# Optimization experiments

Hardware: AMD Instinct MI355X
Metric: run time of the kernel (lower is better)

Reference implementation:

```python
import jax, jax.numpy as jnp
import numpy as np

N, H, L, S, E, D = 2, 8, 2048, 2048, 64, 64
C, K, BITS, ITERS = 128, 32, 32, 10
TEMP = 1.0 / np.sqrt(E)  # softmax_temp default 1/sqrt(E)


def setup_inputs() -> dict:
    key = jax.random.key(0)
    k1, k2, k3, k4 = jax.random.split(key, 4)
    return {
        "queries": jax.random.normal(k1, (N, L, H, E), jnp.float32),
        "keys": jax.random.normal(k2, (N, S, H, E), jnp.float32),
        "values": jax.random.normal(k3, (N, S, H, D), jnp.float32),
        "planes": jax.random.normal(k4, (BITS, E + 1), jnp.float32),
    }


def _cluster(bits):
    """K-means (Lloyd) on hamming distance over hash bits. bits: [N,H,L,B] in {0,1}."""
    qsum = bits.sum(-1)  # [N,H,L]
    idx0 = jnp.linspace(0, L - 1, C).astype(jnp.int32)  # deterministic centroid init
    cbits0 = bits[:, :, idx0, :]  # [N,H,C,B]

    def assign(cbits):
        # hamming(x,c) = sum(x) + sum(c) - 2*x.c  for 0/1 bits
        d = qsum[..., None] + cbits.sum(-1)[:, :, None, :] \
            - 2.0 * jnp.einsum('nhlb,nhcb->nhlc', bits, cbits)
        return jnp.argmin(d, -1)  # [N,H,L]

    def body(cbits, _):
        cl = assign(cbits)
        oh = jax.nn.one_hot(cl, C, dtype=bits.dtype)       # [N,H,L,C]
        counts = oh.sum(2)                                  # [N,H,C]
        bs = jnp.einsum('nhlc,nhlb->nhcb', oh, bits)        # per-cluster bit sums
        newc = (2.0 * bs > counts[..., None]).astype(bits.dtype)  # majority vote
        newc = jnp.where(counts[..., None] > 0, newc, cbits)      # keep empty clusters
        return newc, None

    cbits, _ = jax.lax.scan(body, cbits0, None, length=ITERS)
    cl = assign(cbits)
    counts = jax.nn.one_hot(cl, C, dtype=jnp.float32).sum(2)
    return cl, counts


def reference(queries, keys, values, planes):
    q = queries.transpose(0, 2, 1, 3)  # [N,H,L,E]
    k = keys.transpose(0, 2, 1, 3)     # [N,H,S,E]
    v = values.transpose(0, 2, 1, 3)   # [N,H,S,D]

    # LSH hashing of queries
    proj = jnp.einsum('nhle,be->nhlb', q, planes[:, :E]) + planes[:, E]
    bits = (proj > 0).astype(jnp.float32)
    cl, counts = _cluster(bits)  # [N,H,L], [N,H,C]

    sorted_indx = jnp.argsort(cl, axis=-1)
    sorted_cl = jnp.take_along_axis(cl, sorted_indx, -1)
    sq = jnp.take_along_axis(q, sorted_indx[..., None], 2)  # queries sorted by cluster

    # grouped queries = per-cluster mean
    counts_safe = jnp.maximum(counts, 1.0)
    oh = jax.nn.one_hot(cl, C, dtype=q.dtype)
    Qg = jnp.einsum('nhlc,nhle->nhce', oh, q) / counts_safe[..., None]

    # centroid-key dot products and top-k key selection per cluster
    QK = jnp.einsum('nhce,nhse->nhcs', Qg, k)  # [N,H,C,S]
    topk_values, topk = jax.lax.top_k(QK, K)   # [N,H,C,K]

    # bottom-k attention (dense per-cluster, top-k positions zeroed)
    A_full = jax.nn.softmax(TEMP * QK, -1)
    iN = jnp.arange(N)[:, None, None, None]
    iH = jnp.arange(H)[None, :, None, None]
    iC = jnp.arange(C)[None, None, :, None]
    mask = jnp.zeros_like(QK).at[iN, iH, iC, topk].set(1.0)
    A_b = A_full * (1.0 - mask)
    A_bottomk = A_b.sum(-1)                              # [N,H,C]
    Vb_g = jnp.einsum('nhcs,nhsd->nhcd', A_b, v)         # [N,H,C,D]
    Vb = jnp.take_along_axis(Vb_g, sorted_cl[..., None], 2)   # broadcast to queries
    A_bk_q = jnp.take_along_axis(A_bottomk, sorted_cl, 2)     # [N,H,L]

    # exact top-k attention per query
    topk_q = jnp.take_along_axis(topk, sorted_cl[..., None], 2)  # [N,H,L,K]
    gather = jax.vmap(jax.vmap(lambda t, i: t[i]))  # over N,H
    K_sel = gather(k, topk_q)  # [N,H,L,K,E]
    V_sel = gather(v, topk_q)  # [N,H,L,K,D]
    QKs = jnp.einsum('nhle,nhlke->nhlk', sq, K_sel)
    inf_mask = jnp.isinf(topk_values[:, 0, 0, :])  # [N,K] (padding sentinel; all False here)
    QKs = jnp.where(inf_mask[:, None, None, :], -jnp.inf, QKs)
    A_s = jax.nn.softmax(TEMP * QKs, -1) * (1.0 - A_bk_q[..., None])
    Vt = jnp.einsum('nhlk,nhlkd->nhld', A_s, V_sel)

    # combine and undo the cluster sort
    Vs = Vt + Vb
    rev = jnp.argsort(sorted_indx, -1)
    V_new = jnp.take_along_axis(Vs, rev[..., None], 2)
    sparse_index = jnp.take_along_axis(topk_q, rev[..., None], 2)
    A_topk = jnp.take_along_axis(A_s, rev[..., None], 2)
    return V_new.transpose(0, 2, 1, 3), sparse_index, A_topk
```

## Files before the change

### kernel.cpp

```cpp
#include <hip/hip_runtime.h>
#include <math.h>

constexpr int cN = 2, cH = 8, cL = 2048, cS = 2048, cE = 64, cD = 64;
constexpr int cC = 128, cK = 32, cB = 32, cIT = 10;
constexpr int cNH = cN * cH;
constexpr int SK = 8;
constexpr int CHUNK = cS / SK;
constexpr int NT = 8;
constexpr int HW = cC * 33;
constexpr int NBUF = cIT + 1;

__global__ __launch_bounds__(256)
void k_bits(const float* __restrict__ q, const float* __restrict__ planes,
            unsigned int* __restrict__ bits, int* __restrict__ ghist)
{
    __shared__ float pl[cB * 68];
    int tid = threadIdx.x;
    for (int i = tid; i < cB * (cE + 1); i += 256) {
        int b = i / 65, e = i % 65;
        pl[b * 68 + e] = planes[i];
    }
    {
        const int ZS = NBUF * cNH * HW / 128;
        for (int i = tid; i < ZS; i += 256) ghist[(size_t)blockIdx.x * ZS + i] = 0;
    }
    __syncthreads();
    int idx = blockIdx.x * 256 + tid;
    int l = idx % cL, h = (idx / cL) % cH, n = idx / (cL * cH);
    const float* qr = q + (((size_t)n * cL + l) * cH + h) * cE;
    float qv[cE];
#pragma unroll
    for (int e4 = 0; e4 < cE / 4; ++e4) {
        float4 f = ((const float4*)qr)[e4];
        qv[4*e4+0] = f.x; qv[4*e4+1] = f.y; qv[4*e4+2] = f.z; qv[4*e4+3] = f.w;
    }
    unsigned int w = 0;
    for (int b = 0; b < cB; ++b) {
        const float4* pr = (const float4*)(pl + b * 68);
        float acc = 0.f;
#pragma unroll
        for (int e4 = 0; e4 < cE / 4; ++e4) {
            float4 f = pr[e4];
            acc = fmaf(qv[4*e4+0], f.x, acc);
            acc = fmaf(qv[4*e4+1], f.y, acc);
            acc = fmaf(qv[4*e4+2], f.z, acc);
            acc = fmaf(qv[4*e4+3], f.w, acc);
        }
        acc += pl[b * 68 + 64];
        if (acc > 0.f) w |= (1u << b);
    }
    bits[idx] = w;
}

__global__ __launch_bounds__(256)
void k_lloyd(const unsigned int* __restrict__ bits, int* __restrict__ ghist,
             unsigned int* __restrict__ cents, int* __restrict__ cl,
             int* __restrict__ pcounts, int it)
{
    __shared__ unsigned int scb[cC] __attribute__((aligned(16)));
    __shared__ int hist[HW];
    int tid = threadIdx.x, lane = tid & 63;
    int tile = blockIdx.x & (NT - 1), nh = blockIdx.x / NT;
    if (it == 0) {
        if (tid < cC) {
            int i0 = (int)(((double)tid * 2047.0) / 127.0);
            scb[tid] = bits[(size_t)nh * cL + i0];
        }
    } else {
        const unsigned int* cp = cents + (size_t)(it - 1) * cNH * cC + nh * cC;
        const int* gb = ghist + (size_t)((it - 1) * cNH + nh) * HW;
        if (tid < cC) {
            unsigned int oldc = cp[tid];
            int cnt = gb[4096 + tid];
            if (cnt > 0) {
                unsigned int nw = 0;
#pragma unroll
                for (int b = 0; b < cB; ++b)
                    if (2 * gb[tid * 32 + b] > cnt) nw |= (1u << b);
                oldc = nw;
            }
            scb[tid] = oldc;
        }
    }
    if (it < cIT) {
        for (int i = tid; i < HW; i += 256) hist[i] = 0;
    } else {
        if (tid < cC) hist[4096 + tid] = 0;
    }
    int l = tile * 256 + tid;
    unsigned int w = bits[(size_t)nh * cL + l];
    unsigned long long mymb = 0ull;
    if (it < cIT) {
#pragma unroll
        for (int b = 0; b < cB; ++b) {
            unsigned long long m = __ballot((w >> b) & 1u);
            if ((lane & 31) == b) mymb = m;
        }
    }
    __syncthreads();
    if (tile == 0 && it < cIT && tid < cC)
        cents[(size_t)it * cNH * cC + nh * cC + tid] = scb[tid];
    const uint4* scb4 = (const uint4*)scb;
    int b0 = 0x7fffffff, b1 = 0x7fffffff, b2 = 0x7fffffff, b3 = 0x7fffffff;
    for (int c4 = 0; c4 < cC / 4; ++c4) {
        uint4 cb = scb4[c4];
        int c = c4 * 4;
        b0 = min(b0, (__popc(w ^ cb.x) << 8) | c);
        b1 = min(b1, (__popc(w ^ cb.y) << 8) | (c + 1));
        b2 = min(b2, (__popc(w ^ cb.z) << 8) | (c + 2));
        b3 = min(b3, (__popc(w ^ cb.w) << 8) | (c + 3));
    }
    int best = min(min(b0, b1), min(b2, b3));
    int bc = best & 255;
    if (it == cIT) cl[(size_t)nh * cL + l] = bc;
    if (it < cIT) {
        unsigned long long rem = ~0ull;
        while (rem) {
            int src = __ffsll((long long)rem) - 1;
            int c = __shfl(bc, src);
            unsigned long long m = __ballot(bc == c);
            if (lane < cB) {
                int contrib = __popcll(m & mymb);
                if (contrib) atomicAdd(&hist[c * 32 + lane], contrib);
            }
            if (lane == 63) atomicAdd(&hist[4096 + c], __popcll(m));
            rem &= ~m;
        }
        __syncthreads();
        int* gb = ghist + (size_t)(it * cNH + nh) * HW;
        for (int i = tid; i < HW; i += 256) {
            int v = hist[i];
            if (v) atomicAdd(&gb[i], v);
        }
    } else {
        unsigned long long rem = ~0ull;
        while (rem) {
            int src = __ffsll((long long)rem) - 1;
            int c = __shfl(bc, src);
            unsigned long long m = __ballot(bc == c);
            if (lane == 63) atomicAdd(&hist[4096 + c], __popcll(m));
            rem &= ~m;
        }
        __syncthreads();
        if (tid < cC) pcounts[(nh * NT + tile) * cC + tid] = hist[4096 + tid];
    }
}

__global__ __launch_bounds__(256)
void k_rank(const int* __restrict__ cl, const int* __restrict__ pcounts,
            int* __restrict__ counts, int* __restrict__ moff,
            int* __restrict__ mlist)
{
    __shared__ int pre[cC];
    __shared__ int scn[cC];
    __shared__ int sbefore[cC];
    __shared__ int wcnt[4][cC];
    int tid = threadIdx.x, lane = tid & 63, wid = tid >> 6;
    int tile = blockIdx.x & (NT - 1), nh = blockIdx.x / NT;
    if (tid < cC) {
        int tot = 0, bef = 0;
        for (int t = 0; t < NT; ++t) {
            int v = pcounts[(nh * NT + t) * cC + tid];
            if (t < tile) bef += v;
            tot += v;
        }
        scn[tid] = tot;
        sbefore[tid] = bef;
    }
    {
        int* wf = &wcnt[0][0];
        for (int i = tid; i < 4 * cC; i += 256) wf[i] = 0;
    }
    __syncthreads();
    if (tid == 0) {
        int run = 0;
        for (int i = 0; i < cC; ++i) { pre[i] = run; run += scn[i]; }
    }
    __syncthreads();
    if (tile == 0) {
        if (tid < cC) {
            counts[nh * cC + tid] = scn[tid];
            moff[nh * cC + tid] = pre[tid];
        }
    }
    int l = tile * 256 + tid;
    int bc = cl[(size_t)nh * cL + l];
    unsigned long long ltmask = (1ull << lane) - 1ull;
    int myrank = 0;
    {
        unsigned long long rem = ~0ull;
        while (rem) {
            int src = __ffsll((long long)rem) - 1;
            int c = __shfl(bc, src);
            unsigned long long m = __ballot(bc == c);
            if (lane == 0) wcnt[wid][c] = __popcll(m);
            if (bc == c) myrank = __popcll(m & ltmask);
            rem &= ~m;
        }
    }
    __syncthreads();
    int off = pre[bc] + sbefore[bc] + myrank;
    for (int w2 = 0; w2 < 4; ++w2)
        if (w2 < wid) off += wcnt[w2][bc];
    mlist[(size_t)nh * cL + off] = l;
}

__global__ __launch_bounds__(64)
void k_qg(const float* __restrict__ q, const int* __restrict__ mlist,
          const int* __restrict__ moff, const int* __restrict__ counts,
          float* __restrict__ Qg)
{
    int b = blockIdx.x;
    int nh = b >> 7;
    int h = nh % cH, n = nh / cH;
    int lane = threadIdx.x;
    int off = moff[b];
    int cnt = counts[b];
    const int* ml = mlist + (size_t)nh * cL + off;
    const float* qb = q + ((size_t)n * cL * cH + h) * cE + lane;
    float acc = 0.f;
    int j = 0;
    for (; j + 4 <= cnt; j += 4) {
        int i0 = ml[j], i1 = ml[j + 1], i2 = ml[j + 2], i3 = ml[j + 3];
        float v0 = qb[(size_t)i0 * cH * cE];
        float v1 = qb[(size_t)i1 * cH * cE];
        float v2 = qb[(size_t)i2 * cH * cE];
        float v3 = qb[(size_t)i3 * cH * cE];
        acc += v0; acc += v1; acc += v2; acc += v3;
    }
    for (; j < cnt; ++j) acc += qb[(size_t)ml[j] * cH * cE];
    float cs = (float)(cnt > 0 ? cnt : 1);
    Qg[(size_t)b * cE + lane] = acc / cs;
}

__global__ __launch_bounds__(256)
void k_qk_gemm(const float* __restrict__ key, const float* __restrict__ Qg,
               float* __restrict__ QK)
{
    __shared__ float qgT[cE][cC + 2];
    __shared__ float kT[cE][128 + 2];
    int tid = threadIdx.x;
    int bs = blockIdx.x & 15;
    int nh = blockIdx.x >> 4;
    int h = nh % cH, n = nh / cH;
    const float4* qsrc = (const float4*)(Qg + (size_t)nh * cC * cE);
#pragma unroll
    for (int i = 0; i < 8; ++i) {
        int f = tid + 256 * i;
        int c = f >> 4, e4 = (f & 15) << 2;
        float4 v = qsrc[f];
        qgT[e4+0][c] = v.x; qgT[e4+1][c] = v.y; qgT[e4+2][c] = v.z; qgT[e4+3][c] = v.w;
    }
    const float* kb = key + (size_t)n * cS * cH * cE + (size_t)h * cE;
    int s0 = bs * 128;
#pragma unroll
    for (int i = 0; i < 8; ++i) {
        int f = tid + 256 * i;
        int s = f >> 4, e4 = (f & 15) << 2;
        float4 v = *(const float4*)(kb + (size_t)(s0 + s) * (cH * cE) + e4);
        kT[e4+0][s] = v.x; kT[e4+1][s] = v.y; kT[e4+2][s] = v.z; kT[e4+3][s] = v.w;
    }
    __syncthreads();
    int tx = tid & 15, ty = tid >> 4;
    float acc[8][8];
#pragma unroll
    for (int i = 0; i < 8; ++i)
#pragma unroll
        for (int j = 0; j < 8; ++j) acc[i][j] = 0.f;
    for (int e = 0; e < cE; ++e) {
        float qv[8], kv[8];
#pragma unroll
        for (int i = 0; i < 8; ++i) qv[i] = qgT[e][ty + 16 * i];
#pragma unroll
        for (int j = 0; j < 8; ++j) kv[j] = kT[e][tx + 16 * j];
#pragma unroll
        for (int i = 0; i < 8; ++i)
#pragma unroll
            for (int j = 0; j < 8; ++j)
                acc[i][j] = fmaf(qv[i], kv[j], acc[i][j]);
    }
    float* dst = QK + (size_t)nh * cC * cS + s0;
#pragma unroll
    for (int i = 0; i < 8; ++i)
#pragma unroll
        for (int j = 0; j < 8; ++j)
            dst[(size_t)(ty + 16 * i) * cS + tx + 16 * j] = acc[i][j];
}

__global__ __launch_bounds__(256)
void k_sel(float* __restrict__ QK, int* __restrict__ topk,
           float* __restrict__ abk)
{
    __shared__ int sbins[4 * 257];
    __shared__ int ired[4];
    __shared__ float fred[4];
    __shared__ unsigned skey[cK];
    __shared__ float sval[cK];
    __shared__ int sidx[cK];
    __shared__ int stopk[cK];
    __shared__ int sDig, sRem, scnt;
    __shared__ float sM;
    int tid = threadIdx.x, lane = tid & 63, wid = tid >> 6;
    int b = blockIdx.x;
    float* qrow = QK + (size_t)b * cS;
    float v[8]; unsigned key[8];
#pragma unroll
    for (int j = 0; j < 8; ++j) {
        float f = qrow[tid + j * 256];
        v[j] = f;
        unsigned u = __float_as_uint(f);
        key[j] = (u & 0x80000000u) ? ~u : (u | 0x80000000u);
    }
    if (tid == 0) { sRem = cK; scnt = 0; }
    unsigned pfx = 0;
    for (int pass = 0; pass < 4; ++pass) {
        int sh = 24 - 8 * pass;
        for (int i = tid; i < 4 * 257; i += 256) sbins[i] = 0;
        __syncthreads();
        int rem = sRem;
#pragma unroll
        for (int j = 0; j < 8; ++j) {
            bool cand = (pass == 0) || ((key[j] >> (sh + 8)) == pfx);
            if (cand) atomicAdd(&sbins[wid * 257 + ((key[j] >> sh) & 255)], 1);
        }
        __syncthreads();
        if (wid == 0) {
            int d0 = lane * 4;
            int c0 = sbins[d0] + sbins[257 + d0] + sbins[514 + d0] + sbins[771 + d0];
            int c1 = sbins[d0+1] + sbins[257+d0+1] + sbins[514+d0+1] + sbins[771+d0+1];
            int c2 = sbins[d0+2] + sbins[257+d0+2] + sbins[514+d0+2] + sbins[771+d0+2];
            int c3 = sbins[d0+3] + sbins[257+d0+3] + sbins[514+d0+3] + sbins[771+d0+3];
            int tot = c0 + c1 + c2 + c3;
            int incl = tot;
#pragma unroll
            for (int off = 1; off < 64; off <<= 1) {
                int o = __shfl_down(incl, off);
                if (lane + off < 64) incl += o;
            }
            int sufHi = incl - tot;
            int G3 = sufHi, G2 = sufHi + c3, G1 = G2 + c2, G0 = G1 + c1;
            int hit = -1, hG = 0;
            if (G0 < rem && rem <= G0 + c0) { hit = d0 + 0; hG = G0; }
            if (G1 < rem && rem <= G1 + c1) { hit = d0 + 1; hG = G1; }
            if (G2 < rem && rem <= G2 + c2) { hit = d0 + 2; hG = G2; }
            if (G3 < rem && rem <= G3 + c3) { hit = d0 + 3; hG = G3; }
            unsigned long long m = __ballot(hit >= 0);
            int src = __ffsll((long long)m) - 1;
            int dsel = __shfl(hit, src);
            int Gsel = __shfl(hG, src);
            if (lane == 0) { sDig = dsel; sRem = rem - Gsel; }
        }
        __syncthreads();
        pfx = (pfx << 8) | (unsigned)sDig;
    }
    unsigned T = pfx;
    int need = sRem;
    int myT = 0;
#pragma unroll
    for (int j = 0; j < 8; ++j) myT += (key[j] == T);
#pragma unroll
    for (int off = 1; off < 64; off <<= 1) myT += __shfl_xor(myT, off);
    if (lane == 0) ired[wid] = myT;
    __syncthreads();
    int tieTot = ((ired[0] + ired[1]) + ired[2]) + ired[3];
    int tieCut = 0x7fffffff;
    if (tieTot != need) {
        int last = -1;
        for (int t = 0; t < need; ++t) {
            int mymin = 0x7fffffff;
#pragma unroll
            for (int j = 0; j < 8; ++j) {
                int idx = tid + j * 256;
                if (key[j] == T && idx > last) mymin = min(mymin, idx);
            }
#pragma unroll
            for (int off = 1; off < 64; off <<= 1)
                mymin = min(mymin, __shfl_xor(mymin, off));
            __syncthreads();
            if (lane == 0) ired[wid] = mymin;
            __syncthreads();
            last = min(min(ired[0], ired[1]), min(ired[2], ired[3]));
        }
        tieCut = last;
    }
    __syncthreads();
    int selm = 0;
#pragma unroll
    for (int j = 0; j < 8; ++j) {
        int idx = tid + j * 256;
        bool s_ = (key[j] > T) || (key[j] == T && idx <= tieCut);
        if (s_) {
            int slot = atomicAdd(&scnt, 1);
            skey[slot] = key[j]; sidx[slot] = idx; sval[slot] = v[j];
            selm |= (1 << j);
        }
    }
    __syncthreads();
    if (tid < cK) {
        unsigned kt = skey[tid]; int it = sidx[tid];
        int rank = 0;
#pragma unroll
        for (int j = 0; j < cK; ++j)
            rank += (skey[j] > kt) || (skey[j] == kt && sidx[j] < it);
        stopk[rank] = it;
        if (rank == 0) sM = sval[tid];
    }
    __syncthreads();
    if (tid < cK) topk[(size_t)b * cK + tid] = stopk[tid];
    float M = sM;
    float e8[8]; float ps = 0.f;
#pragma unroll
    for (int j = 0; j < 8; ++j) { e8[j] = expf(0.125f * (v[j] - M)); ps += e8[j]; }
#pragma unroll
    for (int off = 1; off < 64; off <<= 1) ps += __shfl_xor(ps, off);
    if (lane == 0) fred[wid] = ps;
    __syncthreads();
    float den = ((fred[0] + fred[1]) + fred[2]) + fred[3];
    float ab = 0.f;
#pragma unroll
    for (int j = 0; j < 8; ++j) {
        float P = (selm & (1 << j)) ? 0.f : e8[j] / den;
        ab += P;
        qrow[tid + j * 256] = P;
    }
#pragma unroll
    for (int off = 1; off < 64; off <<= 1) ab += __shfl_xor(ab, off);
    __syncthreads();
    if (lane == 0) fred[wid] = ab;
    __syncthreads();
    if (tid == 0) abk[b] = ((fred[0] + fred[1]) + fred[2]) + fred[3];
}

__global__ __launch_bounds__(256)
void k_pv(const float* __restrict__ P, const float* __restrict__ val,
          float* __restrict__ part)
{
    __shared__ float pT[64][64 + 2];
    __shared__ float vT[64][cD + 4];
    int tid = threadIdx.x;
    int ch = blockIdx.x & 1;
    int sk = (blockIdx.x >> 1) & 7;
    int nh = blockIdx.x >> 4;
    int h = nh % cH, n = nh / cH;
    int tx = tid & 15, ty = tid >> 4;
    float acc[4][4];
#pragma unroll
    for (int i = 0; i < 4; ++i)
#pragma unroll
        for (int j = 0; j < 4; ++j) acc[i][j] = 0.f;
    const float* pb = P + ((size_t)nh * cC + ch * 64) * cS;
    const float* vb = val + (size_t)n * cS * cH * cD + (size_t)h * cD;
    for (int sub = 0; sub < CHUNK / 64; ++sub) {
        int s0 = sk * CHUNK + sub * 64;
#pragma unroll
        for (int i = 0; i < 4; ++i) {
            int f = tid + 256 * i;
            int c = f >> 4, s4 = (f & 15) << 2;
            float4 v = *(const float4*)(pb + (size_t)c * cS + s0 + s4);
            pT[c][s4+0] = v.x; pT[c][s4+1] = v.y; pT[c][s4+2] = v.z; pT[c][s4+3] = v.w;
        }
#pragma unroll
        for (int i = 0; i < 4; ++i) {
            int f = tid + 256 * i;
            int ss = f >> 4, d4 = (f & 15) << 2;
            float4 v = *(const float4*)(vb + (size_t)(s0 + ss) * (cH * cD) + d4);
            vT[ss][d4+0] = v.x; vT[ss][d4+1] = v.y; vT[ss][d4+2] = v.z; vT[ss][d4+3] = v.w;
        }
        __syncthreads();
        for (int ss = 0; ss < 64; ++ss) {
            float pv[4];
#pragma unroll
            for (int i = 0; i < 4; ++i) pv[i] = pT[ty + 16 * i][ss];
            float4 vv = *(const float4*)&vT[ss][tx * 4];
#pragma unroll
            for (int i = 0; i < 4; ++i) {
                acc[i][0] = fmaf(pv[i], vv.x, acc[i][0]);
                acc[i][1] = fmaf(pv[i], vv.y, acc[i][1]);
                acc[i][2] = fmaf(pv[i], vv.z, acc[i][2]);
                acc[i][3] = fmaf(pv[i], vv.w, acc[i][3]);
            }
        }
        __syncthreads();
    }
    float* dst = part + (((size_t)sk * cNH + nh) * cC + ch * 64) * cD;
#pragma unroll
    for (int i = 0; i < 4; ++i) {
        float4 o; o.x = acc[i][0]; o.y = acc[i][1]; o.z = acc[i][2]; o.w = acc[i][3];
        *(float4*)(dst + (size_t)(ty + 16 * i) * cD + tx * 4) = o;
    }
}

__global__ __launch_bounds__(256)
void k_out(const float* __restrict__ q, const float* __restrict__ key,
           const float* __restrict__ val, const int* __restrict__ mlist,
           const int* __restrict__ moff, const int* __restrict__ counts,
           const float* __restrict__ abk, const float* __restrict__ part,
           const int* __restrict__ topk, float* __restrict__ out)
{
    __shared__ float vlds[cK][cD + 1];
    __shared__ float aslds[4][cK];
    __shared__ int   st[cK];
    int tid = threadIdx.x, lane = tid & 63, wid = tid >> 6;
    int b = blockIdx.x;
    int nh = b >> 7;
    int h = nh % cH, n = nh / cH;
    if (tid < cK) st[tid] = topk[(size_t)b * cK + tid];
    __syncthreads();
    const float* kb = key + ((size_t)n * cS * cH + h) * cE;
    const float* vb = val + ((size_t)n * cS * cH + h) * cD;
    for (int r = wid; r < cK; r += 4)
        vlds[r][lane] = vb[(size_t)st[r] * cH * cD + lane];
    int k = lane >> 1, hh = lane & 1;
    float4 kreg[8];
    {
        const float* kr = kb + (size_t)st[k] * cH * cE + hh * 32;
#pragma unroll
        for (int j = 0; j < 8; ++j) kreg[j] = ((const float4*)kr)[j];
    }
    float vbgd = 0.f;
    {
        const float* pp = part + (size_t)b * cD + lane;
#pragma unroll
        for (int sk = 0; sk < SK; ++sk)
            vbgd += pp[(size_t)sk * (cNH * cC * cD)];
    }
    __syncthreads();
    int cnt = counts[b];
    int off = moff[b];
    float scale = 1.0f - abk[b];
    float stf = (lane < cK) ? (float)st[lane] : 0.f;
    const int* ml = mlist + (size_t)nh * cL + off;
    const size_t off1 = (size_t)cN * cL * cH * cD;
    const size_t off2 = off1 + (size_t)cN * cH * cL * cK;
    for (int m = wid; m < cnt; m += 4) {
        int l = ml[m];
        const float* qrow = q + (((size_t)n * cL + l) * cH + h) * cE + hh * 32;
        float4 qf[8];
#pragma unroll
        for (int j = 0; j < 8; ++j) qf[j] = ((const float4*)qrow)[j];
        float partial = 0.f;
#pragma unroll
        for (int j = 0; j < 8; ++j) {
            partial = fmaf(qf[j].x, kreg[j].x, partial);
            partial = fmaf(qf[j].y, kreg[j].y, partial);
            partial = fmaf(qf[j].z, kreg[j].z, partial);
            partial = fmaf(qf[j].w, kreg[j].w, partial);
        }
        float qk = partial + __shfl_xor(partial, 1);
        float M = qk;
#pragma unroll
        for (int o = 2; o < 64; o <<= 1) M = fmaxf(M, __shfl_xor(M, o));
        float ev = expf(0.125f * (qk - M));
        float den = ev;
#pragma unroll
        for (int o = 2; o < 64; o <<= 1) den += __shfl_xor(den, o);
        float as_ = (ev / den) * scale;
        if (!hh) aslds[wid][k] = as_;
        float acc = 0.f;
#pragma unroll
        for (int j = 0; j < cK; ++j)
            acc = fmaf(aslds[wid][j], vlds[j][lane], acc);
        acc += vbgd;
        int qidx = nh * cL + l;
        out[(((size_t)n * cL + l) * cH + h) * cD + lane] = acc;
        if (lane < cK) {
            out[off1 + (size_t)qidx * cK + lane] = stf;
            out[off2 + (size_t)qidx * cK + lane] = aslds[wid][lane];
        }
    }
}

extern "C" void kernel_launch(void* const* d_in, const int* in_sizes, int n_in,
                              void* d_out, int out_size, void* d_ws, size_t ws_size,
                              hipStream_t stream)
{
    (void)in_sizes; (void)n_in; (void)out_size; (void)ws_size;
    const float* q      = (const float*)d_in[0];
    const float* key    = (const float*)d_in[1];
    const float* val    = (const float*)d_in[2];
    const float* planes = (const float*)d_in[3];
    char* w = (char*)d_ws;
    unsigned int* bits = (unsigned int*)w;  w += (size_t)cN * cH * cL * 4;
    int*   cl     = (int*)w;                w += (size_t)cN * cH * cL * 4;
    int*   counts = (int*)w;                w += (size_t)cN * cH * cC * 4;
    float* abk    = (float*)w;              w += (size_t)cN * cH * cC * 4;
    float* Qg     = (float*)w;              w += (size_t)cN * cH * cC * cE * 4;
    int*   topkp  = (int*)w;                w += (size_t)cN * cH * cC * cK * 4;
    float* QK     = (float*)w;              w += (size_t)cNH * cC * cS * 4;
    float* part   = (float*)w;              w += (size_t)SK * cNH * cC * cD * 4;
    int*   ghist  = (int*)w;                w += (size_t)NBUF * cNH * HW * 4;
    unsigned int* cents = (unsigned int*)w; w += (size_t)NBUF * cNH * cC * 4;
    int*   pcounts= (int*)w;                w += (size_t)cNH * NT * cC * 4;
    int*   mlist  = (int*)w;                w += (size_t)cNH * cL * 4;
    int*   moff   = (int*)w;                w += (size_t)cNH * cC * 4;
    float* out = (float*)d_out;

    k_bits <<<(cN * cH * cL) / 256, 256, 0, stream>>>(q, planes, bits, ghist);
    for (int it = 0; it <= cIT; ++it)
        k_lloyd <<<cNH * NT, 256, 0, stream>>>(bits, ghist, cents, cl, pcounts, it);
    k_rank <<<cNH * NT, 256, 0, stream>>>(cl, pcounts, counts, moff, mlist);
    k_qg     <<<cNH * cC, 64, 0, stream>>>(q, mlist, moff, counts, Qg);
    k_qk_gemm<<<cNH * 16, 256, 0, stream>>>(key, Qg, QK);
    k_sel    <<<cNH * cC, 256, 0, stream>>>(QK, topkp, abk);
    k_pv     <<<cNH * SK * 2, 256, 0, stream>>>(QK, val, part);
    k_out    <<<cNH * cC, 256, 0, stream>>>(q, key, val, mlist, moff, counts,
                                            abk, part, topkp, out);
}
```

Before: 274.5 us.

## Fuse hashing, Lloyd iterations and ranking into one kernel with grid barriers

Merges the bit-hashing kernel, the eleven per-iteration Lloyd launches and the rank kernel into a single persistent kernel. Per-head tile blocks synchronise through atomic counters with sleep-spin barriers. Centroids and cluster ids stay in shared memory and registers, so the cents and cl buffers go away. This removes about a dozen kernel launches and their global round trips. The cost is spin-wait barriers, which need all 128 blocks resident at once and add a small zeroing launch.

```diff
diff --git a/kernel.cpp b/kernel.cpp
--- a/kernel.cpp
+++ b/kernel.cpp
@@ -8,14 +8,44 @@
 constexpr int CHUNK = cS / SK;
 constexpr int NT = 8;
 constexpr int HW = cC * 33;
-constexpr int NBUF = cIT + 1;
+constexpr int NBUF = cIT;
 
 __global__ __launch_bounds__(256)
-void k_bits(const float* __restrict__ q, const float* __restrict__ planes,
-            unsigned int* __restrict__ bits, int* __restrict__ ghist)
+void k_zero(int* __restrict__ bar)
+{
+    bar[threadIdx.x] = 0;
+}
+
+__global__ __launch_bounds__(256)
+void k_cluster(const float* __restrict__ q, const float* __restrict__ planes,
+               unsigned int* __restrict__ bits, int* __restrict__ ghist,
+               int* __restrict__ pcounts, int* __restrict__ counts,
+               int* __restrict__ moff, int* __restrict__ mlist,
+               int* __restrict__ bar)
 {
     __shared__ float pl[cB * 68];
-    int tid = threadIdx.x;
+    __shared__ unsigned int scb[cC] __attribute__((aligned(16)));
+    __shared__ int hist[HW];
+    int tid = threadIdx.x, lane = tid & 63, wid = tid >> 6;
+    int tile = blockIdx.x & (NT - 1), nh = blockIdx.x / NT;
+    int h = nh % cH, n = nh / cH;
+    int l = tile * 256 + tid;
+    int ep = 0;
+    int* mybar = &bar[nh * 16];
+    auto BARRIER = [&]() {
+        __syncthreads();
+        __threadfence();
+        ++ep;
+        if (tid == 0) {
+            atomicAdd(mybar, 1);
+            int tgt = ep * NT;
+            while (atomicAdd(mybar, 0) < tgt)
+                __builtin_amdgcn_s_sleep(2);
+        }
+        __syncthreads();
+        __threadfence();
+    };
+
     for (int i = tid; i < cB * (cE + 1); i += 256) {
         int b = i / 65, e = i % 65;
         pl[b * 68 + e] = planes[i];
@@ -25,138 +55,112 @@
         for (int i = tid; i < ZS; i += 256) ghist[(size_t)blockIdx.x * ZS + i] = 0;
     }
     __syncthreads();
-    int idx = blockIdx.x * 256 + tid;
-    int l = idx % cL, h = (idx / cL) % cH, n = idx / (cL * cH);
-    const float* qr = q + (((size_t)n * cL + l) * cH + h) * cE;
-    float qv[cE];
-#pragma unroll
-    for (int e4 = 0; e4 < cE / 4; ++e4) {
-        float4 f = ((const float4*)qr)[e4];
-        qv[4*e4+0] = f.x; qv[4*e4+1] = f.y; qv[4*e4+2] = f.z; qv[4*e4+3] = f.w;
-    }
     unsigned int w = 0;
+    {
+        const float* qr = q + (((size_t)n * cL + l) * cH + h) * cE;
+        float qv[cE];
+#pragma unroll
+        for (int e4 = 0; e4 < cE / 4; ++e4) {
+            float4 f = ((const float4*)qr)[e4];
+            qv[4*e4+0] = f.x; qv[4*e4+1] = f.y; qv[4*e4+2] = f.z; qv[4*e4+3] = f.w;
+        }
+        for (int b = 0; b < cB; ++b) {
+            const float4* pr = (const float4*)(pl + b * 68);
+            float acc = 0.f;
+#pragma unroll
+            for (int e4 = 0; e4 < cE / 4; ++e4) {
+                float4 f = pr[e4];
+                acc = fmaf(qv[4*e4+0], f.x, acc);
+                acc = fmaf(qv[4*e4+1], f.y, acc);
+                acc = fmaf(qv[4*e4+2], f.z, acc);
+                acc = fmaf(qv[4*e4+3], f.w, acc);
+            }
+            acc += pl[b * 68 + 64];
+            if (acc > 0.f) w |= (1u << b);
+        }
+    }
+    bits[(size_t)nh * cL + l] = w;
+    unsigned long long mymb = 0ull;
+#pragma unroll
     for (int b = 0; b < cB; ++b) {
-        const float4* pr = (const float4*)(pl + b * 68);
-        float acc = 0.f;
-#pragma unroll
-        for (int e4 = 0; e4 < cE / 4; ++e4) {
-            float4 f = pr[e4];
-            acc = fmaf(qv[4*e4+0], f.x, acc);
-            acc = fmaf(qv[4*e4+1], f.y, acc);
-            acc = fmaf(qv[4*e4+2], f.z, acc);
-            acc = fmaf(qv[4*e4+3], f.w, acc);
-        }
-        acc += pl[b * 68 + 64];
-        if (acc > 0.f) w |= (1u << b);
-    }
-    bits[idx] = w;
-}
-
-__global__ __launch_bounds__(256)
-void k_lloyd(const unsigned int* __restrict__ bits, int* __restrict__ ghist,
-             unsigned int* __restrict__ cents, int* __restrict__ cl,
-             int* __restrict__ pcounts, int it)
-{
-    __shared__ unsigned int scb[cC] __attribute__((aligned(16)));
-    __shared__ int hist[HW];
-    int tid = threadIdx.x, lane = tid & 63;
-    int tile = blockIdx.x & (NT - 1), nh = blockIdx.x / NT;
-    if (it == 0) {
-        if (tid < cC) {
-            int i0 = (int)(((double)tid * 2047.0) / 127.0);
-            scb[tid] = bits[(size_t)nh * cL + i0];
-        }
-    } else {
-        const unsigned int* cp = cents + (size_t)(it - 1) * cNH * cC + nh * cC;
-        const int* gb = ghist + (size_t)((it - 1) * cNH + nh) * HW;
-        if (tid < cC) {
-            unsigned int oldc = cp[tid];
-            int cnt = gb[4096 + tid];
-            if (cnt > 0) {
-                unsigned int nw = 0;
-#pragma unroll
-                for (int b = 0; b < cB; ++b)
-                    if (2 * gb[tid * 32 + b] > cnt) nw |= (1u << b);
-                oldc = nw;
-            }
-            scb[tid] = oldc;
-        }
-    }
-    if (it < cIT) {
-        for (int i = tid; i < HW; i += 256) hist[i] = 0;
-    } else {
-        if (tid < cC) hist[4096 + tid] = 0;
-    }
-    int l = tile * 256 + tid;
-    unsigned int w = bits[(size_t)nh * cL + l];
-    unsigned long long mymb = 0ull;
-    if (it < cIT) {
-#pragma unroll
-        for (int b = 0; b < cB; ++b) {
-            unsigned long long m = __ballot((w >> b) & 1u);
-            if ((lane & 31) == b) mymb = m;
-        }
-    }
-    __syncthreads();
-    if (tile == 0 && it < cIT && tid < cC)
-        cents[(size_t)it * cNH * cC + nh * cC + tid] = scb[tid];
-    const uint4* scb4 = (const uint4*)scb;
-    int b0 = 0x7fffffff, b1 = 0x7fffffff, b2 = 0x7fffffff, b3 = 0x7fffffff;
-    for (int c4 = 0; c4 < cC / 4; ++c4) {
-        uint4 cb = scb4[c4];
-        int c = c4 * 4;
-        b0 = min(b0, (__popc(w ^ cb.x) << 8) | c);
-        b1 = min(b1, (__popc(w ^ cb.y) << 8) | (c + 1));
-        b2 = min(b2, (__popc(w ^ cb.z) << 8) | (c + 2));
-        b3 = min(b3, (__popc(w ^ cb.w) << 8) | (c + 3));
-    }
-    int best = min(min(b0, b1), min(b2, b3));
-    int bc = best & 255;
-    if (it == cIT) cl[(size_t)nh * cL + l] = bc;
-    if (it < cIT) {
-        unsigned long long rem = ~0ull;
-        while (rem) {
-            int src = __ffsll((long long)rem) - 1;
-            int c = __shfl(bc, src);
-            unsigned long long m = __ballot(bc == c);
-            if (lane < cB) {
-                int contrib = __popcll(m & mymb);
-                if (contrib) atomicAdd(&hist[c * 32 + lane], contrib);
-            }
-            if (lane == 63) atomicAdd(&hist[4096 + c], __popcll(m));
-            rem &= ~m;
-        }
-        __syncthreads();
-        int* gb = ghist + (size_t)(it * cNH + nh) * HW;
-        for (int i = tid; i < HW; i += 256) {
-            int v = hist[i];
-            if (v) atomicAdd(&gb[i], v);
-        }
-    } else {
-        unsigned long long rem = ~0ull;
-        while (rem) {
-            int src = __ffsll((long long)rem) - 1;
-            int c = __shfl(bc, src);
-            unsigned long long m = __ballot(bc == c);
-            if (lane == 63) atomicAdd(&hist[4096 + c], __popcll(m));
-            rem &= ~m;
-        }
-        __syncthreads();
-        if (tid < cC) pcounts[(nh * NT + tile) * cC + tid] = hist[4096 + tid];
-    }
-}
-
-__global__ __launch_bounds__(256)
-void k_rank(const int* __restrict__ cl, const int* __restrict__ pcounts,
-            int* __restrict__ counts, int* __restrict__ moff,
-            int* __restrict__ mlist)
-{
-    __shared__ int pre[cC];
-    __shared__ int scn[cC];
-    __shared__ int sbefore[cC];
-    __shared__ int wcnt[4][cC];
-    int tid = threadIdx.x, lane = tid & 63, wid = tid >> 6;
-    int tile = blockIdx.x & (NT - 1), nh = blockIdx.x / NT;
+        unsigned long long m = __ballot((w >> b) & 1u);
+        if ((lane & 31) == b) mymb = m;
+    }
+    BARRIER();
+
+    if (tid < cC) {
+        int i0 = (int)(((double)tid * 2047.0) / 127.0);
+        scb[tid] = bits[(size_t)nh * cL + i0];
+    }
+    int bc = 0;
+    for (int it = 0; it <= cIT; ++it) {
+        if (it < cIT) {
+            for (int i = tid; i < HW; i += 256) hist[i] = 0;
+        } else if (tid < cC) {
+            hist[4096 + tid] = 0;
+        }
+        __syncthreads();
+        const uint4* scb4 = (const uint4*)scb;
+        int b0 = 0x7fffffff, b1 = 0x7fffffff, b2 = 0x7fffffff, b3 = 0x7fffffff;
+        for (int c4 = 0; c4 < cC / 4; ++c4) {
+            uint4 cb = scb4[c4];
+            int c = c4 * 4;
+            b0 = min(b0, (__popc(w ^ cb.x) << 8) | c);
+            b1 = min(b1, (__popc(w ^ cb.y) << 8) | (c + 1));
+            b2 = min(b2, (__popc(w ^ cb.z) << 8) | (c + 2));
+            b3 = min(b3, (__popc(w ^ cb.w) << 8) | (c + 3));
+        }
+        int best = min(min(b0, b1), min(b2, b3));
+        bc = best & 255;
+        if (it < cIT) {
+            unsigned long long rem = ~0ull;
+            while (rem) {
+                int src = __ffsll((long long)rem) - 1;
+                int c = __shfl(bc, src);
+                unsigned long long m = __ballot(bc == c);
+                if (lane < cB) {
+                    int contrib = __popcll(m & mymb);
+                    if (contrib) atomicAdd(&hist[c * 32 + lane], contrib);
+                }
+                if (lane == 63) atomicAdd(&hist[4096 + c], __popcll(m));
+                rem &= ~m;
+            }
+            __syncthreads();
+            int* gb = ghist + (size_t)(it * cNH + nh) * HW;
+            for (int i = tid; i < HW; i += 256) {
+                int v = hist[i];
+                if (v) atomicAdd(&gb[i], v);
+            }
+            BARRIER();
+            if (tid < cC) {
+                const int* gb2 = ghist + (size_t)(it * cNH + nh) * HW;
+                int cnt = gb2[4096 + tid];
+                if (cnt > 0) {
+                    unsigned int nw = 0;
+#pragma unroll
+                    for (int b = 0; b < cB; ++b)
+                        if (2 * gb2[tid * 32 + b] > cnt) nw |= (1u << b);
+                    scb[tid] = nw;
+                }
+            }
+        } else {
+            unsigned long long rem = ~0ull;
+            while (rem) {
+                int src = __ffsll((long long)rem) - 1;
+                int c = __shfl(bc, src);
+                unsigned long long m = __ballot(bc == c);
+                if (lane == 63) atomicAdd(&hist[4096 + c], __popcll(m));
+                rem &= ~m;
+            }
+            __syncthreads();
+            if (tid < cC) pcounts[(nh * NT + tile) * cC + tid] = hist[4096 + tid];
+            BARRIER();
+        }
+    }
+    int* pre = hist;
+    int* sbf = hist + 128;
+    int* scn = hist + 256;
+    int* wcf = hist + 384;
     if (tid < cC) {
         int tot = 0, bef = 0;
         for (int t = 0; t < NT; ++t) {
@@ -165,26 +169,19 @@
             tot += v;
         }
         scn[tid] = tot;
-        sbefore[tid] = bef;
-    }
-    {
-        int* wf = &wcnt[0][0];
-        for (int i = tid; i < 4 * cC; i += 256) wf[i] = 0;
-    }
+        sbf[tid] = bef;
+    }
+    for (int i = tid; i < 4 * cC; i += 256) wcf[i] = 0;
     __syncthreads();
     if (tid == 0) {
         int run = 0;
         for (int i = 0; i < cC; ++i) { pre[i] = run; run += scn[i]; }
     }
     __syncthreads();
-    if (tile == 0) {
-        if (tid < cC) {
-            counts[nh * cC + tid] = scn[tid];
-            moff[nh * cC + tid] = pre[tid];
-        }
-    }
-    int l = tile * 256 + tid;
-    int bc = cl[(size_t)nh * cL + l];
+    if (tile == 0 && tid < cC) {
+        counts[nh * cC + tid] = scn[tid];
+        moff[nh * cC + tid] = pre[tid];
+    }
     unsigned long long ltmask = (1ull << lane) - 1ull;
     int myrank = 0;
     {
@@ -193,15 +190,15 @@
             int src = __ffsll((long long)rem) - 1;
             int c = __shfl(bc, src);
             unsigned long long m = __ballot(bc == c);
-            if (lane == 0) wcnt[wid][c] = __popcll(m);
+            if (lane == 0) wcf[wid * cC + c] = __popcll(m);
             if (bc == c) myrank = __popcll(m & ltmask);
             rem &= ~m;
         }
     }
     __syncthreads();
-    int off = pre[bc] + sbefore[bc] + myrank;
+    int off = pre[bc] + sbf[bc] + myrank;
     for (int w2 = 0; w2 < 4; ++w2)
-        if (w2 < wid) off += wcnt[w2][bc];
+        if (w2 < wid) off += wcf[w2 * cC + bc];
     mlist[(size_t)nh * cL + off] = l;
 }
 
@@ -581,7 +578,6 @@
     const float* planes = (const float*)d_in[3];
     char* w = (char*)d_ws;
     unsigned int* bits = (unsigned int*)w;  w += (size_t)cN * cH * cL * 4;
-    int*   cl     = (int*)w;                w += (size_t)cN * cH * cL * 4;
     int*   counts = (int*)w;                w += (size_t)cN * cH * cC * 4;
     float* abk    = (float*)w;              w += (size_t)cN * cH * cC * 4;
     float* Qg     = (float*)w;              w += (size_t)cN * cH * cC * cE * 4;
@@ -589,16 +585,15 @@
     float* QK     = (float*)w;              w += (size_t)cNH * cC * cS * 4;
     float* part   = (float*)w;              w += (size_t)SK * cNH * cC * cD * 4;
     int*   ghist  = (int*)w;                w += (size_t)NBUF * cNH * HW * 4;
-    unsigned int* cents = (unsigned int*)w; w += (size_t)NBUF * cNH * cC * 4;
     int*   pcounts= (int*)w;                w += (size_t)cNH * NT * cC * 4;
     int*   mlist  = (int*)w;                w += (size_t)cNH * cL * 4;
     int*   moff   = (int*)w;                w += (size_t)cNH * cC * 4;
+    int*   bar    = (int*)w;                w += (size_t)256 * 4;
     float* out = (float*)d_out;
 
-    k_bits <<<(cN * cH * cL) / 256, 256, 0, stream>>>(q, planes, bits, ghist);
-    for (int it = 0; it <= cIT; ++it)
-        k_lloyd <<<cNH * NT, 256, 0, stream>>>(bits, ghist, cents, cl, pcounts, it);
-    k_rank <<<cNH * NT, 256, 0, stream>>>(cl, pcounts, counts, moff, mlist);
+    k_zero   <<<1, 256, 0, stream>>>(bar);
+    k_cluster<<<cNH * NT, 256, 0, stream>>>(q, planes, bits, ghist, pcounts,
+                                            counts, moff, mlist, bar);
     k_qg     <<<cNH * cC, 64, 0, stream>>>(q, mlist, moff, counts, Qg);
     k_qk_gemm<<<cNH * 16, 256, 0, stream>>>(key, Qg, QK);
     k_sel    <<<cNH * cC, 256, 0, stream>>>(QK, topkp, abk);
```

New measurement: 410.1 us. 1.49x slower.
